# Kernel optimization log

Hardware: AMD Instinct MI355X
Metric: run time of the kernel (lower is better)

Reference implementation:

```python
import jax, jax.numpy as jnp
import numpy as np

D_MODEL = 1024
NUM_HEADS = 16
D_K = D_MODEL // NUM_HEADS
ROPE_THETA = 10000.0


def apply_rope(x, positions):
    # x: [b, h, s, d_k]; positions: [b, s] int
    half = x.shape[-1] // 2
    inv_freq = 1.0 / (ROPE_THETA ** (jnp.arange(half, dtype=jnp.float32) * 2.0 / x.shape[-1]))
    ang = positions.astype(jnp.float32)[..., None] * inv_freq  # [b, s, half]
    cos = jnp.cos(ang)[:, None, :, :]  # [b, 1, s, half]
    sin = jnp.sin(ang)[:, None, :, :]
    x1 = x[..., 0::2]
    x2 = x[..., 1::2]
    r1 = x1 * cos - x2 * sin
    r2 = x1 * sin + x2 * cos
    # interleave back
    out = jnp.stack([r1, r2], axis=-1).reshape(x.shape)
    return out


def setup_inputs() -> dict:
    key = jax.random.key(0)
    k1, k2, k3 = jax.random.split(key, 3)
    b, s = 4, 2048
    x = jax.random.normal(k1, (b, s, D_MODEL), dtype=jnp.float32)
    token_positions = jnp.broadcast_to(jnp.arange(s, dtype=jnp.int32), (b, s))
    w_qkv = jax.random.normal(k2, (3 * D_MODEL, D_MODEL), dtype=jnp.float32) * (D_MODEL ** -0.5)
    w_o = jax.random.normal(k3, (D_MODEL, D_MODEL), dtype=jnp.float32) * (D_MODEL ** -0.5)
    return {"x": x, "token_positions": token_positions, "w_qkv": w_qkv, "w_o": w_o}


def reference(x, token_positions, w_qkv, w_o):
    b, s, _ = x.shape
    qkv = jnp.einsum('bsd,ed->bse', x, w_qkv)  # [b, s, 3*H*Dk]
    qkv = qkv.reshape(b, s, 3, NUM_HEADS, D_K).transpose(2, 0, 3, 1, 4)  # [3, b, H, s, Dk]
    q, k, v = qkv[0], qkv[1], qkv[2]
    q = apply_rope(q, token_positions)
    k = apply_rope(k, token_positions)
    scale = 1.0 / jnp.sqrt(jnp.float32(D_K))
    scores = jnp.einsum('bhqd,bhkd->bhqk', q, k) * scale
    causal = jnp.tril(jnp.ones((s, s), dtype=bool))
    scores = jnp.where(causal, scores, -jnp.inf)
    attn = jax.nn.softmax(scores, axis=-1)
    out = jnp.einsum('bhqk,bhkd->bhqd', attn, v)  # [b, H, s, Dk]
    out = out.transpose(0, 2, 1, 3).reshape(b, s, D_MODEL)
    return jnp.einsum('bse,de->bsd', out, w_o)
```

## Files before the change

### kernel.cpp

```cpp
#include <hip/hip_runtime.h>
#include <math.h>

typedef __bf16 bf16x8 __attribute__((ext_vector_type(8)));
typedef __bf16 bf16x4 __attribute__((ext_vector_type(4)));
typedef float  floatx4 __attribute__((ext_vector_type(4)));
typedef unsigned short ushortx8 __attribute__((ext_vector_type(8)));

#define D_MODEL 1024
#define NQKV 3072
#define SEQ 2048
#define BATCH 4
#define NH 16
#define DKD 64
#define MTOT (BATCH*SEQ)

#define SCALE_L2E 0.18033688011112042f
#define FIXED_M 16.0f

__device__ __forceinline__ unsigned short f2bf(float f) {
  unsigned int u = __float_as_uint(f);
  u += 0x7FFFu + ((u >> 16) & 1u);
  return (unsigned short)(u >> 16);
}

__device__ __forceinline__ float dpp_swap1(float v) {
  int i = __builtin_amdgcn_mov_dpp(__float_as_int(v), 0xB1, 0xF, 0xF, true);
  return __int_as_float(i);
}

__device__ __forceinline__ void gld16(unsigned short* lds, const unsigned short* g) {
  __builtin_amdgcn_global_load_lds(
      (const __attribute__((address_space(1))) unsigned int*)g,
      (__attribute__((address_space(3))) unsigned int*)lds, 16, 0, 0);
}

__global__ void cvt3_kernel(const float4* __restrict__ a, ushort4* __restrict__ ao, int na4,
                            const float4* __restrict__ b, ushort4* __restrict__ bo, int nb4,
                            const float4* __restrict__ c, ushort4* __restrict__ co, int nc4)
{
  int i = blockIdx.x * blockDim.x + threadIdx.x;
  const float4* in; ushort4* out; int j;
  if (i < na4)            { in = a; out = ao; j = i; }
  else if (i < na4 + nb4) { in = b; out = bo; j = i - na4; }
  else if (i < na4 + nb4 + nc4) { in = c; out = co; j = i - na4 - nb4; }
  else return;
  float4 v = in[j];
  ushort4 o;
  o.x = f2bf(v.x); o.y = f2bf(v.y); o.z = f2bf(v.z); o.w = f2bf(v.w);
  out[j] = o;
}

template<int EPI>
__global__ __launch_bounds__(256) void gemm_bt(
    const unsigned short* __restrict__ A,
    const unsigned short* __restrict__ B,
    float* __restrict__ C, int K, int N,
    const int* __restrict__ pos,
    unsigned short* __restrict__ qb,
    unsigned short* __restrict__ kb,
    unsigned short* __restrict__ vb)
{
  __shared__ unsigned short As[128*64];
  __shared__ unsigned short Bs[128*64];
  const int tid = threadIdx.x;
  const int wave = tid >> 6, lane = tid & 63;
  const int l16 = lane & 15, quad = lane >> 4;
  const int wr = wave >> 1, wc = wave & 1;
  const int bm = blockIdx.x * 128, bn = blockIdx.y * 128;

  floatx4 acc[4][4] = {};

  int offA[4], offB[4];
#pragma unroll
  for (int u = 0; u < 4; ++u) {
    int task = tid + u*256;
    int row = task >> 3;
    int c   = (task & 7) ^ (row & 7);
    offA[u] = (bm + row) * K + c*8;
    offB[u] = (bn + row) * K + c*8;
  }
  unsigned short* Al = &As[tid * 8];
  unsigned short* Bl = &Bs[tid * 8];
  const int x0 = ((quad)     ^ (l16 & 7)) * 8;
  const int x1 = ((4 + quad) ^ (l16 & 7)) * 8;

  for (int k0 = 0; k0 < K; k0 += 64) {
    __syncthreads();
#pragma unroll
    for (int u = 0; u < 4; ++u) {
      gld16(Al + u*2048, A + offA[u] + k0);
      gld16(Bl + u*2048, B + offB[u] + k0);
    }
    __syncthreads();
#pragma unroll
    for (int kk = 0; kk < 2; ++kk) {
      const int xo = kk ? x1 : x0;
      bf16x8 a[4], b[4];
#pragma unroll
      for (int i = 0; i < 4; ++i) a[i] = *(const bf16x8*)&As[(wr*64 + i*16 + l16)*64 + xo];
#pragma unroll
      for (int t = 0; t < 4; ++t) b[t] = *(const bf16x8*)&Bs[(wc*64 + t*16 + l16)*64 + xo];
#pragma unroll
      for (int i = 0; i < 4; ++i)
#pragma unroll
        for (int t = 0; t < 4; ++t)
          acc[i][t] = __builtin_amdgcn_mfma_f32_16x16x32_bf16(a[i], b[t], acc[i][t], 0, 0, 0);
    }
  }

  if (EPI == 0) {
#pragma unroll
    for (int i = 0; i < 4; ++i)
#pragma unroll
      for (int r = 0; r < 4; ++r) {
        int row = bm + wr*64 + i*16 + quad*4 + r;
#pragma unroll
        for (int t = 0; t < 4; ++t) {
          int col = bn + wc*64 + t*16 + l16;
          C[(size_t)row * N + col] = acc[i][t][r];
        }
      }
  } else {
    const int which = bn >> 10;
    int h_t[4], dk_t[4];
#pragma unroll
    for (int t = 0; t < 4; ++t) {
      int col = bn + wc*64 + t*16 + l16;
      h_t[t]  = (col >> 6) & 15;
      dk_t[t] = col & 63;
    }
    if (which == 2) {
#pragma unroll
      for (int i = 0; i < 4; ++i) {
        int row0 = bm + wr*64 + i*16 + quad*4;
        int b = row0 >> 11, s0 = row0 & 2047;
#pragma unroll
        for (int t = 0; t < 4; ++t) {
          union { bf16x4 v; uint2 u; } pk;
#pragma unroll
          for (int r = 0; r < 4; ++r) pk.v[r] = (__bf16)acc[i][t][r];
          *(uint2*)&vb[((size_t)((b << 4) + h_t[t]) * DKD + dk_t[t]) * SEQ + s0] = pk.u;
        }
      }
    } else {
      float inv_t[4];
#pragma unroll
      for (int t = 0; t < 4; ++t)
        inv_t[t] = exp2f((float)(dk_t[t] >> 1) * (-13.287712379549449f / 32.0f));
      unsigned short* dstp = (which == 0) ? qb : kb;
      const float sc_ = (which == 0) ? SCALE_L2E : 1.0f;
      const bool oddl = (lane & 1) != 0;
      const float invA = oddl ? inv_t[2] : inv_t[0];
      const float invB = oddl ? inv_t[3] : inv_t[1];
      const size_t hoA = (size_t)(oddl ? h_t[2] : h_t[0]) * SEQ * DKD
                       + (size_t)((oddl ? dk_t[2] : dk_t[0]) & ~1);
      const size_t hoB = (size_t)(oddl ? h_t[3] : h_t[1]) * SEQ * DKD
                       + (size_t)((oddl ? dk_t[3] : dk_t[1]) & ~1);
#pragma unroll
      for (int i = 0; i < 4; ++i)
#pragma unroll
        for (int r = 0; r < 4; ++r) {
          int row = bm + wr*64 + i*16 + quad*4 + r;
          int b = row >> 11, s = row & 2047;
          float p = (float)pos[row];
          float v0 = acc[i][0][r], v1 = acc[i][1][r];
          float v2 = acc[i][2][r], v3 = acc[i][3][r];
          float q0 = dpp_swap1(v0), q1 = dpp_swap1(v1);
          float q2 = dpp_swap1(v2), q3 = dpp_swap1(v3);
          float evA = oddl ? q2 : v0, odA = oddl ? v2 : q0;
          float evB = oddl ? q3 : v1, odB = oddl ? v3 : q1;
          size_t bs = ((size_t)(b << 4) * SEQ + s) * DKD;
          float snA, csA; __sincosf(p * invA, &snA, &csA);
          csA *= sc_; snA *= sc_;
          union { __bf16 h[2]; unsigned int u; } pkA;
          pkA.h[0] = (__bf16)(evA * csA - odA * snA);
          pkA.h[1] = (__bf16)(evA * snA + odA * csA);
          *(unsigned int*)&dstp[bs + hoA] = pkA.u;
          float snB, csB; __sincosf(p * invB, &snB, &csB);
          csB *= sc_; snB *= sc_;
          union { __bf16 h[2]; unsigned int u; } pkB;
          pkB.h[0] = (__bf16)(evB * csB - odB * snB);
          pkB.h[1] = (__bf16)(evB * snB + odB * csB);
          *(unsigned int*)&dstp[bs + hoB] = pkB.u;
        }
    }
  }
}

__global__ __launch_bounds__(256) void attn_kernel(
    const unsigned short* __restrict__ qb,
    const unsigned short* __restrict__ kb,
    const unsigned short* __restrict__ vb,
    unsigned short* __restrict__ ob)
{
  __shared__ unsigned short Ks[128*64];
  __shared__ unsigned short Vt[64*128];
  __shared__ unsigned short Ps[128*72];
  const int tid = threadIdx.x;
  const int wave = tid >> 6, lane = tid & 63;
  const int l16 = lane & 15, quad = lane >> 4;
  const int l8 = l16 & 7;
  const int id = blockIdx.x;
  const int bh = id & 63;
  const int qtb = 15 - (id >> 6);
  const int qbase = qtb * 128;
  const int rounds = qtb + 1;
  const size_t base = (size_t)bh * SEQ * DKD;
  const int bb = bh >> 4, hh0 = bh & 15;

  bf16x8 vones;
#pragma unroll
  for (int j = 0; j < 8; ++j) vones[j] = (__bf16)1.0f;

  const int kx0 = (quad ^ l8) * 8;
  const int kx1 = ((4 + quad) ^ l8) * 8;

  int ksrc[4], vsrc[4];
#pragma unroll
  for (int u = 0; u < 4; ++u) {
    int task = tid + u*256;
    int kr_ = task >> 3, kc_ = (task & 7) ^ (kr_ & 7);
    ksrc[u] = kr_*DKD + kc_*8;
    int vr_ = task >> 4, vc_ = (task & 15) ^ (vr_ & 7);
    vsrc[u] = vr_*SEQ + vc_*8;
  }

  bf16x8 qf[2][2];
#pragma unroll
  for (int f = 0; f < 2; ++f)
#pragma unroll
    for (int hh = 0; hh < 2; ++hh)
      qf[f][hh] = *(const bf16x8*)&qb[base + (size_t)(qbase + f*64 + wave*16 + l16)*DKD + hh*32 + quad*8];

  floatx4 o[2][4] = {};
  floatx4 ls[2] = {};

  for (int kt = 0; kt < rounds; ++kt) {
    const unsigned short* kg = kb + base + (size_t)kt * 128 * DKD;
    const unsigned short* vg = vb + base + kt * 128;
    __syncthreads();
#pragma unroll
    for (int u = 0; u < 4; ++u) {
      gld16(&Ks[(tid + u*256)*8], kg + ksrc[u]);
      gld16(&Vt[(tid + u*256)*8], vg + vsrc[u]);
    }
    __syncthreads();
    const bool diag = (kt == rounds - 1);
#pragma unroll
    for (int ch = 0; ch < 2; ++ch) {
      floatx4 sc[2][4];
#pragma unroll
      for (int f = 0; f < 2; ++f)
#pragma unroll
        for (int tl = 0; tl < 4; ++tl)
          sc[f][tl] = (floatx4){-FIXED_M, -FIXED_M, -FIXED_M, -FIXED_M};
#pragma unroll
      for (int tl = 0; tl < 4; ++tl) {
        int t = ch*4 + tl;
        const int krow = (t*16 + l16)*64;
        bf16x8 ka0 = *(const bf16x8*)&Ks[krow + kx0];
        bf16x8 ka1 = *(const bf16x8*)&Ks[krow + kx1];
        sc[0][tl] = __builtin_amdgcn_mfma_f32_16x16x32_bf16(ka0, qf[0][0], sc[0][tl], 0, 0, 0);
        sc[0][tl] = __builtin_amdgcn_mfma_f32_16x16x32_bf16(ka1, qf[0][1], sc[0][tl], 0, 0, 0);
        sc[1][tl] = __builtin_amdgcn_mfma_f32_16x16x32_bf16(ka0, qf[1][0], sc[1][tl], 0, 0, 0);
        sc[1][tl] = __builtin_amdgcn_mfma_f32_16x16x32_bf16(ka1, qf[1][1], sc[1][tl], 0, 0, 0);
      }
#pragma unroll
      for (int f = 0; f < 2; ++f) {
        const int qrl = f*64 + wave*16 + l16;
#pragma unroll
        for (int tl = 0; tl < 4; ++tl) {
          int t = ch*4 + tl;
          union { bf16x4 v; uint2 u; } pk;
#pragma unroll
          for (int r = 0; r < 4; ++r) {
            float s = sc[f][tl][r];
            if (diag && (t*16 + quad*4 + r > qrl)) s = -INFINITY;
            pk.v[r] = (__bf16)__builtin_amdgcn_exp2f(s);
          }
          *(uint2*)&Ps[(f*64 + wave*16 + l16)*72 + tl*16 + quad*4] = pk.u;
        }
      }
      bf16x8 pf[2][2];
#pragma unroll
      for (int f = 0; f < 2; ++f)
#pragma unroll
        for (int cl = 0; cl < 2; ++cl)
          pf[f][cl] = *(const bf16x8*)&Ps[(f*64 + wave*16 + l16)*72 + cl*32 + quad*8];
#pragma unroll
      for (int cl = 0; cl < 2; ++cl) {
        int c = ch*2 + cl;
        __builtin_amdgcn_s_setprio(1);
#pragma unroll
        for (int t = 0; t < 4; ++t) {
          int d = t*16 + l16;
          bf16x8 vf = *(const bf16x8*)&Vt[d*128 + (((c*4 + quad) ^ l8) * 8)];
          o[0][t] = __builtin_amdgcn_mfma_f32_16x16x32_bf16(vf, pf[0][cl], o[0][t], 0, 0, 0);
          o[1][t] = __builtin_amdgcn_mfma_f32_16x16x32_bf16(vf, pf[1][cl], o[1][t], 0, 0, 0);
        }
        ls[0] = __builtin_amdgcn_mfma_f32_16x16x32_bf16(vones, pf[0][cl], ls[0], 0, 0, 0);
        ls[1] = __builtin_amdgcn_mfma_f32_16x16x32_bf16(vones, pf[1][cl], ls[1], 0, 0, 0);
        __builtin_amdgcn_s_setprio(0);
      }
    }
  }

#pragma unroll
  for (int f = 0; f < 2; ++f) {
    int qrow = qbase + f*64 + wave*16 + l16;
    float invl = 1.0f / ls[f][0];
    size_t rb = ((size_t)bb * SEQ + qrow) * D_MODEL + hh0*DKD;
#pragma unroll
    for (int t = 0; t < 4; ++t) {
      union { bf16x4 v; uint2 u; } pk;
#pragma unroll
      for (int r = 0; r < 4; ++r) pk.v[r] = (__bf16)(o[f][t][r] * invl);
      *(uint2*)&ob[rb + t*16 + quad*4] = pk.u;
    }
  }
}

extern "C" void kernel_launch(void* const* d_in, const int* in_sizes, int n_in,
                              void* d_out, int out_size, void* d_ws, size_t ws_size,
                              hipStream_t stream) {
  const float* x    = (const float*)d_in[0];
  const int*   pos  = (const int*)d_in[1];
  const float* wqkv = (const float*)d_in[2];
  const float* wo   = (const float*)d_in[3];

  char* ws = (char*)d_ws;
  unsigned short* xb    = (unsigned short*)(ws);
  unsigned short* wqkvb = (unsigned short*)(ws + 16777216);
  unsigned short* wob   = (unsigned short*)(ws + 23068672);
  unsigned short* qb    = (unsigned short*)(ws + 25165824);
  unsigned short* kb    = (unsigned short*)(ws + 41943040);
  unsigned short* vb    = (unsigned short*)(ws + 58720256);
  unsigned short* ab    = (unsigned short*)(ws + 75497472);

  int nx  = MTOT * D_MODEL;
  int nwq = NQKV * D_MODEL;
  int nwo = D_MODEL * D_MODEL;
  int n4tot = nx/4 + nwq/4 + nwo/4;
  cvt3_kernel<<<(n4tot + 255)/256, 256, 0, stream>>>(
      (const float4*)x, (ushort4*)xb, nx/4,
      (const float4*)wqkv, (ushort4*)wqkvb, nwq/4,
      (const float4*)wo, (ushort4*)wob, nwo/4);

  gemm_bt<1><<<dim3(MTOT/128, NQKV/128), 256, 0, stream>>>(
      xb, wqkvb, (float*)nullptr, D_MODEL, NQKV, pos, qb, kb, vb);

  attn_kernel<<<dim3(1024), 256, 0, stream>>>(qb, kb, vb, ab);

  gemm_bt<0><<<dim3(MTOT/128, D_MODEL/128), 256, 0, stream>>>(
      ab, wob, (float*)d_out, D_MODEL, D_MODEL, nullptr, nullptr, nullptr, nullptr);
}
```

Baseline: 237.3 us.

## Triple-buffer GEMM LDS tiles with K=32 stages and async prefetch

Reworks the bf16 GEMM main loop from single-buffered K=64 tiles with two barriers per step into a three-stage ring of K=32 LDS buffers. Two stages are prefetched ahead, and partial vmcnt waits plus one barrier per iteration let global-to-LDS loads overlap the MFMA work. The swizzle changes to a 4-chunk XOR to fit the narrower rows. In exchange there are more loop iterations with less MFMA work each, 48KB of LDS per block, and correctness depends on the hand-written waitcnt counts.

```diff
diff --git a/kernel.cpp b/kernel.cpp
--- a/kernel.cpp
+++ b/kernel.cpp
@@ -60,8 +60,8 @@
     unsigned short* __restrict__ kb,
     unsigned short* __restrict__ vb)
 {
-  __shared__ unsigned short As[128*64];
-  __shared__ unsigned short Bs[128*64];
+  __shared__ unsigned short As[3][128*32];
+  __shared__ unsigned short Bs[3][128*32];
   const int tid = threadIdx.x;
   const int wave = tid >> 6, lane = tid & 63;
   const int l16 = lane & 15, quad = lane >> 4;
@@ -70,42 +70,58 @@
 
   floatx4 acc[4][4] = {};
 
-  int offA[4], offB[4];
-#pragma unroll
-  for (int u = 0; u < 4; ++u) {
+  int offA[2], offB[2];
+#pragma unroll
+  for (int u = 0; u < 2; ++u) {
     int task = tid + u*256;
-    int row = task >> 3;
-    int c   = (task & 7) ^ (row & 7);
-    offA[u] = (bm + row) * K + c*8;
-    offB[u] = (bn + row) * K + c*8;
-  }
-  unsigned short* Al = &As[tid * 8];
-  unsigned short* Bl = &Bs[tid * 8];
-  const int x0 = ((quad)     ^ (l16 & 7)) * 8;
-  const int x1 = ((4 + quad) ^ (l16 & 7)) * 8;
-
-  for (int k0 = 0; k0 < K; k0 += 64) {
-    __syncthreads();
-#pragma unroll
-    for (int u = 0; u < 4; ++u) {
-      gld16(Al + u*2048, A + offA[u] + k0);
-      gld16(Bl + u*2048, B + offB[u] + k0);
-    }
-    __syncthreads();
-#pragma unroll
-    for (int kk = 0; kk < 2; ++kk) {
-      const int xo = kk ? x1 : x0;
-      bf16x8 a[4], b[4];
-#pragma unroll
-      for (int i = 0; i < 4; ++i) a[i] = *(const bf16x8*)&As[(wr*64 + i*16 + l16)*64 + xo];
-#pragma unroll
-      for (int t = 0; t < 4; ++t) b[t] = *(const bf16x8*)&Bs[(wc*64 + t*16 + l16)*64 + xo];
-#pragma unroll
-      for (int i = 0; i < 4; ++i)
-#pragma unroll
-        for (int t = 0; t < 4; ++t)
-          acc[i][t] = __builtin_amdgcn_mfma_f32_16x16x32_bf16(a[i], b[t], acc[i][t], 0, 0, 0);
-    }
+    int row = task >> 2;
+    int cs  = (task & 3) ^ (row & 3);
+    offA[u] = (bm + row) * K + cs*8;
+    offB[u] = (bn + row) * K + cs*8;
+  }
+  const int ldst = tid * 8;
+  const int xo = (quad ^ (l16 & 3)) * 8;
+
+  unsigned short *a0 = As[0], *a1 = As[1], *a2 = As[2];
+  unsigned short *b0 = Bs[0], *b1 = Bs[1], *b2 = Bs[2];
+
+#pragma unroll
+  for (int u = 0; u < 2; ++u) {
+    gld16(&a0[ldst + u*2048], A + offA[u]);
+    gld16(&b0[ldst + u*2048], B + offB[u]);
+  }
+#pragma unroll
+  for (int u = 0; u < 2; ++u) {
+    gld16(&a1[ldst + u*2048], A + offA[u] + 32);
+    gld16(&b1[ldst + u*2048], B + offB[u] + 32);
+  }
+
+  const int nt = K >> 5;
+  for (int t = 0; t < nt; ++t) {
+    if (t + 1 < nt) { asm volatile("s_waitcnt vmcnt(4)" ::: "memory"); }
+    else            { asm volatile("s_waitcnt vmcnt(0)" ::: "memory"); }
+    __builtin_amdgcn_sched_barrier(0);
+    __builtin_amdgcn_s_barrier();
+    if (t + 2 < nt) {
+      const int k2 = (t + 2) << 5;
+#pragma unroll
+      for (int u = 0; u < 2; ++u) {
+        gld16(&a2[ldst + u*2048], A + offA[u] + k2);
+        gld16(&b2[ldst + u*2048], B + offB[u] + k2);
+      }
+    }
+    bf16x8 a[4], b[4];
+#pragma unroll
+    for (int i = 0; i < 4; ++i) a[i] = *(const bf16x8*)&a0[(wr*64 + i*16 + l16)*32 + xo];
+#pragma unroll
+    for (int tt = 0; tt < 4; ++tt) b[tt] = *(const bf16x8*)&b0[(wc*64 + tt*16 + l16)*32 + xo];
+#pragma unroll
+    for (int i = 0; i < 4; ++i)
+#pragma unroll
+      for (int tt = 0; tt < 4; ++tt)
+        acc[i][tt] = __builtin_amdgcn_mfma_f32_16x16x32_bf16(a[i], b[tt], acc[i][tt], 0, 0, 0);
+    unsigned short* ta = a0; a0 = a1; a1 = a2; a2 = ta;
+    unsigned short* tb = b0; b0 = b1; b1 = b2; b2 = tb;
   }
 
   if (EPI == 0) {
```

New measurement: 251.9 us. +6.1%, slower.
